# Kernel optimization log

Hardware: AMD Instinct MI355X
Metric: run time of the kernel (lower is better)

## Reference

```python
import jax, jax.numpy as jnp
import numpy as np

B, C, H, W, N = 32, 256, 56, 56, 1024


def setup_inputs() -> dict:
    key = jax.random.key(0)
    k1, k2, k3, k4 = jax.random.split(key, 4)
    x = jax.random.normal(k1, (B, C, H, W), dtype=jnp.float32)
    W_s = jax.random.normal(k2, (N, H, W), dtype=jnp.float32)
    W_d = jax.random.normal(k3, (N, C, 1, 1), dtype=jnp.float32)
    W_b = jax.random.normal(k4, (1, N), dtype=jnp.float32)
    return {"x": x, "W_s": W_s, "W_d": W_d, "W_b": W_b}


def reference(x, W_s, W_d, W_b):
    # Original: out = einsum('bchw,nhw->bnchw'); per-neuron 1x1 conv with W_d[n]
    # (C -> 1 channel); sum over (c,h,w); add bias. Mathematically:
    #   out[b,n] = sum_{c,h,w} x[b,c,h,w] * W_s[n,h,w] * W_d[n,c] + W_b[0,n]
    # Computed without materializing the (B,N,C,H,W) blow-up:
    y = jnp.einsum('bchw,nhw->bnc', x, W_s)          # spatial contraction
    out = jnp.einsum('bnc,nc->bn', y, W_d[:, :, 0, 0])  # channel contraction
    return out + W_b
```

## Files before the change

kernel.cpp:

```cpp
#include <hip/hip_runtime.h>
#include <stdint.h>


#define K_DIM 3136
#define N_DIM 1024
#define C_DIM 256
#define B_DIM 32
#define M_DIM 8192
#define X_ELEMS (M_DIM * K_DIM)
#define WS_ELEMS (N_DIM * K_DIM)

typedef __attribute__((ext_vector_type(8))) short short8v;
typedef __attribute__((ext_vector_type(4))) float f32x4;

__device__ __forceinline__ short f2bf(float f) {
  union { float f; unsigned u; } v; v.f = f;
  unsigned r = v.u + 0x7FFFu + ((v.u >> 16) & 1u);
  return (short)(r >> 16);
}

__device__ __forceinline__ void async16(const void* g, void* l) {
  __builtin_amdgcn_global_load_lds(
      (const __attribute__((address_space(1))) unsigned int*)g,
      (__attribute__((address_space(3))) unsigned int*)l, 16, 0, 0);
}

#define XBLK (X_ELEMS / 2048)
#define CVBLK ((X_ELEMS + WS_ELEMS) / 2048)
__global__ __launch_bounds__(256) void convert_bf16_bias(
    const float* __restrict__ x, const float* __restrict__ Ws,
    const float* __restrict__ Wb, short* __restrict__ dst,
    float* __restrict__ out) {
  int bid = blockIdx.x;
  if (bid >= CVBLK) {
    int i = (bid - CVBLK) * 256 + threadIdx.x;
    out[i] = Wb[i & (N_DIM - 1)];
    return;
  }
  const float* src;
  short* d;
  size_t base;
  if (bid < XBLK) {
    src = x; d = dst; base = (size_t)bid * 2048;
  } else {
    src = Ws; d = dst + X_ELEMS; base = (size_t)(bid - XBLK) * 2048;
  }
  size_t i = base + threadIdx.x * 8;
  f32x4 v0 = __builtin_nontemporal_load((const f32x4*)(src + i));
  f32x4 v1 = __builtin_nontemporal_load((const f32x4*)(src + i) + 1);
  short8v s;
  s[0] = f2bf(v0.x); s[1] = f2bf(v0.y); s[2] = f2bf(v0.z); s[3] = f2bf(v0.w);
  s[4] = f2bf(v1.x); s[5] = f2bf(v1.y); s[6] = f2bf(v1.z); s[7] = f2bf(v1.w);
  *(short8v*)(d + i) = s;
}

__global__ __launch_bounds__(512, 4) void gemm_fused(
    const short* __restrict__ Abf, const short* __restrict__ Bbf,
    const float* __restrict__ Wd, float* __restrict__ out) {
  __shared__ __align__(16) short As[256 * 64];
  __shared__ __align__(16) short Bs[128 * 64];

  const int bid = blockIdx.x;
  const int mt = bid & 31;
  const int nt = (bid >> 5) & 7;
  const int z = bid >> 8;
  const int kt0 = z * 25;
  const int ktn = z ? 24 : 25;

  const int t = threadIdx.x;
  const int lane = t & 63;
  const int wv = t >> 6;
  const int r = lane & 15;
  const int q = lane >> 4;
  const int wm = wv >> 1, wn = wv & 1;

  const int rr = lane >> 3;
  const int k8 = (lane & 7) ^ rr;
  const short* Aw = Abf + (size_t)(mt * 256 + wv * 32 + rr) * K_DIM + k8 * 8 + kt0 * 64;
  const short* Bw = Bbf + (size_t)(nt * 128 + wv * 16 + rr) * K_DIM + k8 * 8 + kt0 * 64;
  char* AsB = (char*)As + wv * 4096;
  char* BsB = (char*)Bs + wv * 2048;

  f32x4 acc[4][4];
#pragma unroll
  for (int i = 0; i < 4; ++i)
#pragma unroll
    for (int j = 0; j < 4; ++j) acc[i][j] = (f32x4)0.0f;

  for (int kt = 0; kt < ktn; ++kt) {
    __syncthreads();
#pragma unroll
    for (int p = 0; p < 4; ++p)
      async16(Aw + (size_t)p * 8 * K_DIM + kt * 64, AsB + p * 1024);
#pragma unroll
    for (int p = 0; p < 2; ++p)
      async16(Bw + (size_t)p * 8 * K_DIM + kt * 64, BsB + p * 1024);
    __syncthreads();

#pragma unroll
    for (int ks = 0; ks < 2; ++ks) {
      const int xo = ((ks * 4 + q) ^ (r & 7)) * 16;
      short8v a[4], b[4];
#pragma unroll
      for (int i = 0; i < 4; ++i)
        a[i] = *(const short8v*)((const char*)As + (64 * wm + 16 * i + r) * 128 + xo);
#pragma unroll
      for (int j = 0; j < 4; ++j)
        b[j] = *(const short8v*)((const char*)Bs + (64 * wn + 16 * j + r) * 128 + xo);
#pragma unroll
      for (int i = 0; i < 4; ++i)
#pragma unroll
        for (int j = 0; j < 4; ++j)
          acc[i][j] = __builtin_amdgcn_mfma_f32_16x16x32_bf16(a[i], b[j],
                                                              acc[i][j], 0, 0, 0);
    }
  }

#pragma unroll
  for (int j = 0; j < 4; ++j) {
    const int n_g = nt * 128 + 64 * wn + 16 * j + r;
    float p = 0.0f;
#pragma unroll
    for (int i = 0; i < 4; ++i) {
      const int c_l = 64 * wm + 16 * i + 4 * q;
      const float4 wd = *(const float4*)(Wd + (size_t)n_g * C_DIM + c_l);
      p += acc[i][j].x * wd.x + acc[i][j].y * wd.y + acc[i][j].z * wd.z +
           acc[i][j].w * wd.w;
    }
    p += __shfl_xor(p, 16, 64);
    p += __shfl_xor(p, 32, 64);
    if (q == 0) atomicAdd(&out[(size_t)mt * N_DIM + n_g], p);
  }
}

extern "C" void kernel_launch(void* const* d_in, const int* in_sizes, int n_in,
                              void* d_out, int out_size, void* d_ws, size_t ws_size,
                              hipStream_t stream) {
  const float* x = (const float*)d_in[0];
  const float* Ws = (const float*)d_in[1];
  const float* Wd = (const float*)d_in[2];
  const float* Wb = (const float*)d_in[3];
  float* out = (float*)d_out;
  short* xbf = (short*)d_ws;

  convert_bf16_bias<<<dim3(CVBLK + 128), dim3(256), 0, stream>>>(x, Ws, Wb, xbf, out);
  gemm_fused<<<dim3(32 * 8 * 2), dim3(512), 0, stream>>>(xbf, xbf + X_ELEMS, Wd, out);
}
```

Measured before the change: 209.6 us.

## Fuse fp32-to-bf16 conversion of x into the GEMM A-tile load

Drops the separate pass that converted all of x to bf16 in workspace. The GEMM now reads fp32 x directly, packs pairs to bf16 in registers and writes them into the swizzled LDS tile. Only W_s is still pre-converted, alongside the bias init. This removes a full read and write of x through HBM, but the GEMM now does synchronous global loads instead of async global-to-LDS copies and fetches twice the bytes per A tile. The rounding also changes to round-half-up.

New measurement: 237.1 us. 13.1% more time.

```diff
diff --git a/kernel.cpp b/kernel.cpp
--- a/kernel.cpp
+++ b/kernel.cpp
@@ -7,16 +7,22 @@
 #define C_DIM 256
 #define B_DIM 32
 #define M_DIM 8192
-#define X_ELEMS (M_DIM * K_DIM)
 #define WS_ELEMS (N_DIM * K_DIM)
 
 typedef __attribute__((ext_vector_type(8))) short short8v;
 typedef __attribute__((ext_vector_type(4))) float f32x4;
+typedef __attribute__((ext_vector_type(4))) unsigned int uint4v;
 
 __device__ __forceinline__ short f2bf(float f) {
   union { float f; unsigned u; } v; v.f = f;
   unsigned r = v.u + 0x7FFFu + ((v.u >> 16) & 1u);
   return (short)(r >> 16);
+}
+
+__device__ __forceinline__ unsigned pk2bf(float a, float b) {
+  unsigned ua = __float_as_uint(a) + 0x8000u;
+  unsigned ub = __float_as_uint(b) + 0x8000u;
+  return (ua >> 16) | (ub & 0xFFFF0000u);
 }
 
 __device__ __forceinline__ void async16(const void* g, void* l) {
@@ -25,37 +31,27 @@
       (__attribute__((address_space(3))) unsigned int*)l, 16, 0, 0);
 }
 
-#define XBLK (X_ELEMS / 2048)
-#define CVBLK ((X_ELEMS + WS_ELEMS) / 2048)
-__global__ __launch_bounds__(256) void convert_bf16_bias(
-    const float* __restrict__ x, const float* __restrict__ Ws,
-    const float* __restrict__ Wb, short* __restrict__ dst,
-    float* __restrict__ out) {
+#define WSBLK (WS_ELEMS / 2048)
+__global__ __launch_bounds__(256) void convert_ws_bias(
+    const float* __restrict__ Ws, const float* __restrict__ Wb,
+    short* __restrict__ dst, float* __restrict__ out) {
   int bid = blockIdx.x;
-  if (bid >= CVBLK) {
-    int i = (bid - CVBLK) * 256 + threadIdx.x;
+  if (bid >= WSBLK) {
+    int i = (bid - WSBLK) * 256 + threadIdx.x;
     out[i] = Wb[i & (N_DIM - 1)];
     return;
   }
-  const float* src;
-  short* d;
-  size_t base;
-  if (bid < XBLK) {
-    src = x; d = dst; base = (size_t)bid * 2048;
-  } else {
-    src = Ws; d = dst + X_ELEMS; base = (size_t)(bid - XBLK) * 2048;
-  }
-  size_t i = base + threadIdx.x * 8;
-  f32x4 v0 = __builtin_nontemporal_load((const f32x4*)(src + i));
-  f32x4 v1 = __builtin_nontemporal_load((const f32x4*)(src + i) + 1);
+  size_t i = (size_t)bid * 2048 + threadIdx.x * 8;
+  f32x4 v0 = __builtin_nontemporal_load((const f32x4*)(Ws + i));
+  f32x4 v1 = __builtin_nontemporal_load((const f32x4*)(Ws + i) + 1);
   short8v s;
   s[0] = f2bf(v0.x); s[1] = f2bf(v0.y); s[2] = f2bf(v0.z); s[3] = f2bf(v0.w);
   s[4] = f2bf(v1.x); s[5] = f2bf(v1.y); s[6] = f2bf(v1.z); s[7] = f2bf(v1.w);
-  *(short8v*)(d + i) = s;
+  *(short8v*)(dst + i) = s;
 }
 
 __global__ __launch_bounds__(512, 4) void gemm_fused(
-    const short* __restrict__ Abf, const short* __restrict__ Bbf,
+    const float* __restrict__ x, const short* __restrict__ Bbf,
     const float* __restrict__ Wd, float* __restrict__ out) {
   __shared__ __align__(16) short As[256 * 64];
   __shared__ __align__(16) short Bs[128 * 64];
@@ -76,10 +72,15 @@
 
   const int rr = lane >> 3;
   const int k8 = (lane & 7) ^ rr;
-  const short* Aw = Abf + (size_t)(mt * 256 + wv * 32 + rr) * K_DIM + k8 * 8 + kt0 * 64;
   const short* Bw = Bbf + (size_t)(nt * 128 + wv * 16 + rr) * K_DIM + k8 * 8 + kt0 * 64;
-  char* AsB = (char*)As + wv * 4096;
   char* BsB = (char*)Bs + wv * 2048;
+
+  const int rr8 = lane >> 3;
+  const int c8 = lane & 7;
+  const int slotA = c8 ^ rr8;
+  const float* Aw =
+      x + (size_t)(mt * 256 + wv * 32 + rr8) * K_DIM + kt0 * 64 + c8 * 8;
+  short* AsW = As + (wv * 32 + rr8) * 64 + slotA * 8;
 
   f32x4 acc[4][4];
 #pragma unroll
@@ -90,11 +91,20 @@
   for (int kt = 0; kt < ktn; ++kt) {
     __syncthreads();
 #pragma unroll
-    for (int p = 0; p < 4; ++p)
-      async16(Aw + (size_t)p * 8 * K_DIM + kt * 64, AsB + p * 1024);
-#pragma unroll
     for (int p = 0; p < 2; ++p)
       async16(Bw + (size_t)p * 8 * K_DIM + kt * 64, BsB + p * 1024);
+#pragma unroll
+    for (int w = 0; w < 4; ++w) {
+      const float* g = Aw + (size_t)w * 8 * K_DIM + kt * 64;
+      f32x4 va = *(const f32x4*)g;
+      f32x4 vb = *(const f32x4*)(g + 4);
+      uint4v u;
+      u.x = pk2bf(va.x, va.y);
+      u.y = pk2bf(va.z, va.w);
+      u.z = pk2bf(vb.x, vb.y);
+      u.w = pk2bf(vb.z, vb.w);
+      *(uint4v*)(AsW + (size_t)w * 8 * 64) = u;
+    }
     __syncthreads();
 
 #pragma unroll
@@ -141,8 +151,8 @@
   const float* Wd = (const float*)d_in[2];
   const float* Wb = (const float*)d_in[3];
   float* out = (float*)d_out;
-  short* xbf = (short*)d_ws;
+  short* wsbf = (short*)d_ws;
 
-  convert_bf16_bias<<<dim3(CVBLK + 128), dim3(256), 0, stream>>>(x, Ws, Wb, xbf, out);
-  gemm_fused<<<dim3(32 * 8 * 2), dim3(512), 0, stream>>>(xbf, xbf + X_ELEMS, Wd, out);
+  convert_ws_bias<<<dim3(WSBLK + 128), dim3(256), 0, stream>>>(Ws, Wb, wsbf, out);
+  gemm_fused<<<dim3(32 * 8 * 2), dim3(512), 0, stream>>>(x, wsbf, Wd, out);
 }
```
